# Kernel tuning notes

Measured on AMD Instinct MI355X. Metric: run time of the kernel, lower is better.

## Reference

```python
import jax, jax.numpy as jnp
import numpy as np

CUTOFF = 10.0
K = 32            # max_num_neighbors
NUM_GRAPHS = 64
ATOMS = 128
N = NUM_GRAPHS * ATOMS
HID = 128
FIL = 128
NG = 50           # num_gaussians
LAYERS = 6
MAX_Z = 100
PI = 3.14159265   # constant used verbatim in the torch source


def silu(x):
    return x * jax.nn.sigmoid(x)


def build_graph(pos, batch):
    """Dense cdist + per-node top-K neighbor selection (radius_graph_pure).
    Returns idx[i,k] = k-th nearest neighbor j of center i, and a validity mask.
    Torch edge (row, col) = (j, i): node j receives a message computed from x[i].
    """
    p = jax.lax.stop_gradient(pos)
    d2 = jnp.sum((p[:, None, :] - p[None, :, :]) ** 2, -1)          # [N,N]
    same = batch[:, None] == batch[None, :]
    eye = jnp.eye(p.shape[0], dtype=bool)
    valid = same & (d2 < CUTOFF * CUTOFF) & (~eye)
    dm = jnp.where(valid, d2, jnp.inf)
    neg, idx = jax.lax.top_k(-dm, K)                                 # [N,K]
    return idx, jnp.isfinite(neg)                                    # edge valid iff within mask


def setup_inputs() -> dict:
    key = jax.random.key(0)
    ks = jax.random.split(key, 20)
    s = 0.05
    inp = {
        "pos": jax.random.normal(ks[0], (N, 3), jnp.float32),
        "z": jax.random.randint(ks[1], (N,), 0, MAX_Z),
        "batch": jnp.repeat(jnp.arange(NUM_GRAPHS), ATOMS),
        # parameters (weights stored as [in, out])
        "emb": jax.random.normal(ks[2], (MAX_Z, HID), jnp.float32) * s,
        "mw1": jax.random.normal(ks[3], (LAYERS, NG, FIL), jnp.float32) * s,
        "mb1": jax.random.normal(ks[4], (LAYERS, FIL), jnp.float32) * s,
        "mw2": jax.random.normal(ks[5], (LAYERS, FIL, FIL), jnp.float32) * s,
        "mb2": jax.random.normal(ks[6], (LAYERS, FIL), jnp.float32) * s,
        "l1w": jax.random.normal(ks[7], (LAYERS, HID, FIL), jnp.float32) * s,
        "l1b": jax.random.normal(ks[8], (LAYERS, FIL), jnp.float32) * s,
        "l2w": jax.random.normal(ks[9], (LAYERS, FIL, HID), jnp.float32) * s,
        "l2b": jax.random.normal(ks[10], (LAYERS, HID), jnp.float32) * s,
        "ow1": jax.random.normal(ks[11], (HID, HID // 2), jnp.float32) * s,
        "ob1": jax.random.normal(ks[12], (HID // 2,), jnp.float32) * s,
        "ow2": jax.random.normal(ks[13], (HID // 2, 1), jnp.float32) * s,
        "ob2": jax.random.normal(ks[14], (1,), jnp.float32) * s,
    }
    return inp


def reference(pos, z, batch, emb, mw1, mb1, mw2, mb2, l1w, l1b, l2w, l2b, ow1, ob1, ow2, ob2):
    idx, evalid = build_graph(pos, batch)                 # [N,K], [N,K]
    ev = evalid.astype(pos.dtype)
    diff = pos[idx] - pos[:, None, :]                     # [N,K,3]
    d2e = jnp.sum(diff * diff, -1)
    dist = jnp.sqrt(jnp.where(evalid, d2e, 1.0))          # safe sqrt for masked edges
    offset = jnp.linspace(0.0, CUTOFF, NG)
    width = CUTOFF / (NG - 1)
    rbf = jnp.exp(-0.5 * ((dist[..., None] - offset) / width) ** 2)   # [N,K,NG]
    cval = 0.5 * (jnp.cos(dist * PI / CUTOFF) + 1.0)
    cval = cval * (dist < CUTOFF).astype(pos.dtype) * ev  # zero out invalid edges

    h = emb[z]                                            # [N,HID]
    flat_idx = idx.reshape(-1)                            # receivers (torch row)
    for l in range(LAYERS):
        W = silu(rbf @ mw1[l] + mb1[l]) @ mw2[l] + mb2[l]           # filter MLP
        W = W * cval[..., None]                                       # [N,K,FIL]
        xj = (h @ l1w[l] + l1b[l])[:, None, :]                        # sender = center i
        msg = (xj * W).reshape(N * K, FIL)
        agg = jax.ops.segment_sum(msg, flat_idx, num_segments=N)     # scatter_add at row
        h = h + silu(agg @ l2w[l] + l2b[l])

    out = (silu(h @ ow1 + ob1) @ ow2 + ob2)[:, 0]         # [N]
    return jax.ops.segment_sum(out, batch, num_segments=NUM_GRAPHS)  # [G]
```

## Files before the change

### kernel.cpp

```cpp
#include <hip/hip_runtime.h>
#include <math.h>

typedef unsigned short u16;
typedef unsigned int   u32;
typedef unsigned long long u64;

#define NATOMS 8192
#define GRAPHS 64
#define KNN    32
#define NGAUSS 50
#define HID    128
#define LAYERS 6
#define NTAB   4096
#define SA     136
#define SW1    72
#define SH     132

typedef __attribute__((ext_vector_type(8))) short bf16x8;
typedef __attribute__((ext_vector_type(4))) float f32x4;

__device__ __forceinline__ float bf2f(u16 v) {
    return __uint_as_float(((u32)v) << 16);
}
__device__ __forceinline__ u16 f2bf(float f) {
    u32 u = __float_as_uint(f);
    u32 lsb = (u >> 16) & 1u;
    u += 0x7fffu + lsb;
    return (u16)(u >> 16);
}
__device__ __forceinline__ u32 pkbf(float lo, float hi) {
#if __has_builtin(__builtin_amdgcn_cvt_pk_bf16_f32)
    auto r = __builtin_amdgcn_cvt_pk_bf16_f32(lo, hi);
    u32 u; __builtin_memcpy(&u, &r, 4); return u;
#else
    return (u32)f2bf(lo) | ((u32)f2bf(hi) << 16);
#endif
}
__device__ __forceinline__ float silu_f(float x) {
    return x * __builtin_amdgcn_rcpf(1.0f + __expf(-x));
}
__device__ __forceinline__ bf16x8 ldfrag(const u16* p) {
    return *(const bf16x8*)__builtin_assume_aligned(p, 16);
}
__device__ __forceinline__ u64 shfl_xor_u64(u64 v, int mask) {
    u32 lo = (u32)v, hi = (u32)(v >> 32);
    lo = (u32)__shfl_xor((int)lo, mask, 64);
    hi = (u32)__shfl_xor((int)hi, mask, 64);
    return ((u64)hi << 32) | lo;
}
__device__ __forceinline__ float ldf(const void* p, int i, bool f32in) {
    return f32in ? ((const float*)p)[i] : bf2f(((const u16*)p)[i]);
}
union U8 { bf16x8 v; u32 w[4]; };

__global__ void probe_kernel(const u16* __restrict__ raw, int* __restrict__ flag,
                             int* __restrict__ rev_cnt, float* __restrict__ gsum,
                             int* __restrict__ done_cnt, int* __restrict__ xflags) {
    __shared__ int s;
    int t = threadIdx.x;
    if (t == 0) s = 0;
    __syncthreads();
    float x = bf2f(raw[2 * t]);
    if (!(fabsf(x) < 1000.0f)) atomicOr(&s, 1);
    for (int i = t; i < NATOMS; i += 256) rev_cnt[i] = 0;
    for (int i = t; i < 2048; i += 256) xflags[i] = 0;
    if (t < GRAPHS) gsum[t] = 0.0f;
    if (t == 0) *done_cnt = 0;
    __syncthreads();
    if (t == 0) *flag = s;
}

#define NARR 9
struct IngestDesc {
    const void* src[NARR];
    void*       dst[NARR];
    int         n[NARR];
};

#define NB_BUILD 2048
#define NB_PREP  768

__launch_bounds__(256)
__global__ void setup_kernel(const void* __restrict__ pos,
                             const void* __restrict__ l1w, const void* __restrict__ l2w,
                             u16* __restrict__ l1wt, u16* __restrict__ l2wt,
                             IngestDesc d, int total_ing,
                             const int* __restrict__ flag,
                             int* __restrict__ rev_cnt, u32* __restrict__ rev) {
    int bid = blockIdx.x;
    bool f32in = (*flag != 0);
    if (bid < NB_BUILD) {
        int wv = threadIdx.x >> 6, lane = threadIdx.x & 63;
        int t = bid * 4 + wv;
        int tl = t & 127;
        int base = t & ~127;
        float cx = ldf(pos, t * 3 + 0, f32in);
        float cy = ldf(pos, t * 3 + 1, f32in);
        float cz = ldf(pos, t * 3 + 2, f32in);
        u64 key[2];
#pragma unroll
        for (int c = 0; c < 2; ++c) {
            int j = lane + c * 64;
            float jx = ldf(pos, (base + j) * 3 + 0, f32in);
            float jy = ldf(pos, (base + j) * 3 + 1, f32in);
            float jz = ldf(pos, (base + j) * 3 + 2, f32in);
            float dx = __fsub_rn(cx, jx);
            float dy = __fsub_rn(cy, jy);
            float dz = __fsub_rn(cz, jz);
            float d2 = __fadd_rn(__fadd_rn(__fmul_rn(dx, dx), __fmul_rn(dy, dy)),
                                 __fmul_rn(dz, dz));
            bool valid = (j != tl) && (d2 < 100.0f);
            key[c] = valid ? ((((u64)__float_as_uint(d2)) << 32) | (u32)j) : ~0ULL;
        }
#pragma unroll
        for (int k = 2; k <= 128; k <<= 1) {
#pragma unroll
            for (int j = k >> 1; j > 0; j >>= 1) {
                if (j == 64) {
                    u64 lo = key[0] < key[1] ? key[0] : key[1];
                    u64 hi = key[0] < key[1] ? key[1] : key[0];
                    key[0] = lo; key[1] = hi;
                } else {
#pragma unroll
                    for (int r = 0; r < 2; ++r) {
                        u64 o = shfl_xor_u64(key[r], j);
                        u32 ii = (u32)(r * 64 + lane);
                        bool dir = ((ii & (u32)k) == 0);
                        bool lower = ((ii & (u32)j) == 0);
                        bool keep_min = (dir == lower);
                        bool less = key[r] < o;
                        key[r] = (less == keep_min) ? key[r] : o;
                    }
                }
            }
        }
        if (lane < KNN) {
            u64 m = key[0];
            if (m != ~0ULL) {
                float d2 = __uint_as_float((u32)(m >> 32));
                float dd = __fsqrt_rn(d2);
                if (dd < 10.0f) {
                    float u = dd * ((float)(NTAB - 1) / 10.0f);
                    int i0 = (int)(u + 0.5f);
                    if (i0 > NTAB - 1) i0 = NTAB - 1;
                    int jn = base + (int)(m & 0xffffffffu);
                    int p = atomicAdd(&rev_cnt[jn], 1);
                    rev[(size_t)jn * 128 + p] = ((u32)i0 << 7) | (u32)(t & 127);
                }
            }
        }
    } else if (bid < NB_BUILD + NB_PREP) {
        int gid = (bid - NB_BUILD) * 256 + threadIdx.x;
        int seg = gid / 98304;
        int tt = gid % 98304;
        int l = tt >> 14;
        int n = (tt >> 7) & 127;
        int k = tt & 127;
        const void* src = (seg == 0) ? l1w : l2w;
        u16* dst = (seg == 0) ? l1wt : l2wt;
        int si = l * 16384 + k * 128 + n;
        float v = f32in ? ((const float*)src)[si] : bf2f(((const u16*)src)[si]);
        dst[tt] = f2bf(v);
    } else {
        int gid = (bid - NB_BUILD - NB_PREP) * 256 + threadIdx.x;
        if (gid < total_ing) {
            int a = 0, off = gid;
            while (off >= d.n[a]) { off -= d.n[a]; ++a; }
            float v = f32in ? ((const float*)d.src[a])[off]
                            : bf2f(((const u16*)d.src[a])[off]);
            ((float*)d.dst[a])[off] = v;
        }
    }
}

__launch_bounds__(256)
__global__ void vtab_kernel(const void* __restrict__ mw1,
                            const void* __restrict__ mw2,
                            const float* __restrict__ b1,
                            const float* __restrict__ b2,
                            const int* __restrict__ flag,
                            u32* __restrict__ pk) {
    __shared__ u16 s_t1[128 * SA];
    __shared__ u16 s_w1[128 * SW1];
    __shared__ u16 s_w2[128 * SA];
    int tid = threadIdx.x;
    int l = blockIdx.x / (NTAB / 128);
    int rbase = (blockIdx.x % (NTAB / 128)) * 128;
    {
        bool f32in = (*flag != 0);
#pragma unroll
        for (int p = 0; p < 32; ++p) {
            int idx = p * 256 + tid;
            int k = idx >> 7, n = idx & 127;
            float v = (k < 50) ? ldf(mw1, l * 6400 + k * 128 + n, f32in) : 0.0f;
            s_w1[n * SW1 + k] = f2bf(v);
        }
#pragma unroll
        for (int p = 0; p < 64; ++p) {
            int idx = p * 256 + tid;
            int k = idx >> 7, n = idx & 127;
            s_w2[n * SA + k] = f2bf(ldf(mw2, l * 16384 + k * 128 + n, f32in));
        }
    }
    __syncthreads();

    int wv = tid >> 6, lane = tid & 63;
    int quad = lane >> 4, lr = lane & 15;
    int m0 = wv * 32;

    {
        const float wgi = 49.0f / 10.0f;
        const float dstep = 10.0f / (float)(NTAB - 1);
        U8 afr[2][2];
#pragma unroll
        for (int mt = 0; mt < 2; ++mt) {
            float d = (float)(rbase + m0 + mt * 16 + lr) * dstep;
            float u = d * wgi;
#pragma unroll
            for (int kki = 0; kki < 2; ++kki) {
                float t0 = u - (float)(quad * 8) - (float)(kki * 32);
                float vj[8];
#pragma unroll
                for (int j = 0; j < 8; ++j) {
                    float tt = t0 - (float)j;
                    float e = __expf(-0.5f * tt * tt);
                    if (kki == 1 && (quad * 8 + j) >= 18) e = 0.0f;
                    vj[j] = e;
                }
#pragma unroll
                for (int p = 0; p < 4; ++p)
                    afr[mt][kki].w[p] = pkbf(vj[2 * p], vj[2 * p + 1]);
            }
        }
        f32x4 accA[2][8];
#pragma unroll
        for (int mt = 0; mt < 2; ++mt)
#pragma unroll
            for (int nt = 0; nt < 8; ++nt) accA[mt][nt] = (f32x4){0.f, 0.f, 0.f, 0.f};
#pragma unroll
        for (int kki = 0; kki < 2; ++kki) {
#pragma unroll
            for (int nt = 0; nt < 8; ++nt) {
                bf16x8 b = ldfrag(&s_w1[(nt * 16 + lr) * SW1 + kki * 32 + quad * 8]);
                accA[0][nt] = __builtin_amdgcn_mfma_f32_16x16x32_bf16(afr[0][kki].v, b, accA[0][nt], 0, 0, 0);
                accA[1][nt] = __builtin_amdgcn_mfma_f32_16x16x32_bf16(afr[1][kki].v, b, accA[1][nt], 0, 0, 0);
            }
        }
#pragma unroll
        for (int mt = 0; mt < 2; ++mt) {
            int r0 = m0 + mt * 16 + quad * 4;
            u16* tp0 = &s_t1[r0 * SA + lr];
#pragma unroll
            for (int nt = 0; nt < 8; ++nt) {
                int col = nt * 16;
                float bb = b1[l * 128 + col + lr];
                u32 p01 = pkbf(silu_f(accA[mt][nt][0] + bb),
                               silu_f(accA[mt][nt][1] + bb));
                u32 p23 = pkbf(silu_f(accA[mt][nt][2] + bb),
                               silu_f(accA[mt][nt][3] + bb));
                u16* tp = tp0 + col;
                tp[0]      = (u16)p01;
                tp[SA]     = (u16)(p01 >> 16);
                tp[2 * SA] = (u16)p23;
                tp[3 * SA] = (u16)(p23 >> 16);
            }
        }
    }
    {
        f32x4 accB[2][8];
#pragma unroll
        for (int mt = 0; mt < 2; ++mt)
#pragma unroll
            for (int nt = 0; nt < 8; ++nt) accB[mt][nt] = (f32x4){0.f, 0.f, 0.f, 0.f};
#pragma unroll
        for (int kk = 0; kk < 128; kk += 32) {
            bf16x8 a0 = ldfrag(&s_t1[(m0 + lr)      * SA + kk + quad * 8]);
            bf16x8 a1 = ldfrag(&s_t1[(m0 + 16 + lr) * SA + kk + quad * 8]);
#pragma unroll
            for (int nt = 0; nt < 8; ++nt) {
                bf16x8 b = ldfrag(&s_w2[(nt * 16 + lr) * SA + kk + quad * 8]);
                accB[0][nt] = __builtin_amdgcn_mfma_f32_16x16x32_bf16(a0, b, accB[0][nt], 0, 0, 0);
                accB[1][nt] = __builtin_amdgcn_mfma_f32_16x16x32_bf16(a1, b, accB[1][nt], 0, 0, 0);
            }
        }
        const float dstep = 10.0f / (float)(NTAB - 1);
#pragma unroll
        for (int mt = 0; mt < 2; ++mt) {
            int r0 = m0 + mt * 16 + quad * 4;
            float cv[4];
#pragma unroll
            for (int r = 0; r < 4; ++r) {
                float d = (float)(rbase + r0 + r) * dstep;
                cv[r] = 0.5f * (cosf(d * 3.14159265f / 10.0f) + 1.0f);
            }
#pragma unroll
            for (int nt = 0; nt < 8; ++nt) {
                int col = nt * 16 + lr;
                float bb = b2[l * 128 + col];
#pragma unroll
                for (int r = 0; r < 4; ++r) {
                    float val = (accB[mt][nt][r] + bb) * cv[r];
                    float oth = __shfl_xor(val, 1, 64);
                    if ((lr & 1) == 0) {
                        int row = rbase + r0 + r;
                        pk[((size_t)l * NTAB + row) * 64 + (col >> 1)] =
                            pkbf(val, oth);
                    }
                }
            }
        }
    }
}

#define AGG_ISSUE(T, X, base, ev)                                              \
    {                                                                          \
        _Pragma("unroll") for (int q = 0; q < 8; ++q) {                        \
            int e = (base) + q;                                                \
            u32 pe = __builtin_amdgcn_readlane((ev), e & 63);                  \
            int sy = (int)(pe >> 7);                                           \
            int sx = (int)(pe & 127u);                                         \
            T[q] = pkl[(size_t)sy * 64 + lane];                                \
            X[q] = *(const u32*)&s_x[sx * SA + c2];                            \
        }                                                                      \
    }

#define AGG_COMPUTE(T, X)                                                      \
    {                                                                          \
        _Pragma("unroll") for (int q = 0; q < 8; ++q) {                        \
            float v0 = bf2f((u16)T[q]) * bf2f((u16)X[q]);                      \
            float v1 = bf2f((u16)(T[q] >> 16)) * bf2f((u16)(X[q] >> 16));      \
            switch (q & 3) {                                                   \
                case 0: a0 += v0; a1 += v1; break;                             \
                case 1: b0 += v0; b1v += v1; break;                            \
                case 2: c0 += v0; c1 += v1; break;                             \
                default: d0 += v0; d1 += v1; break;                            \
            }                                                                  \
        }                                                                      \
    }

__launch_bounds__(1024, 1)
__global__ void graph_kernel(const int* __restrict__ rev_cnt,
                             const u32* __restrict__ rev,
                             const u32* __restrict__ pk,
                             const int* __restrict__ z,
                             const float* __restrict__ emb,
                             const u16* __restrict__ l1wt,
                             const float* __restrict__ l1b,
                             const u16* __restrict__ l2wt,
                             const float* __restrict__ l2b,
                             const float* __restrict__ ow1,
                             const float* __restrict__ ob1,
                             const float* __restrict__ ow2,
                             const float* __restrict__ ob2,
                             u32* __restrict__ xbuf,
                             int* __restrict__ xflags,
                             float* __restrict__ gsum,
                             int* __restrict__ done_cnt,
                             void* __restrict__ out,
                             const int* __restrict__ flag) {
    __shared__ __align__(16) u16 s_x[128 * SA];
    __shared__ __align__(16) u16 s_hb[64 * SA];
    __shared__ __align__(16) u16 s_pair[2 * 64 * SA];
    __shared__ float s_b1[128], s_b2[128];
    __shared__ float s_sum;
    __shared__ int s_last;

    u16* s_ahi = s_pair;
    u16* s_alo = s_pair + 64 * SA;

    int tid = threadIdx.x;
    int bid = blockIdx.x;
    int g = bid & 63, q4 = bid >> 6;
    int abase = g * 128;
    int rbase = q4 * 32;
    int w = tid >> 6, lane = tid & 63;
    int quad = lane >> 4, lr = lane & 15;
    int rowt = (w >> 3) * 16;
    int coln = (w & 7) * 16;
    int c2 = lane * 2;

    float hreg[4];

    u32* xb_own[2] = {xbuf + ((size_t)bid * 2 + 0) * 2048,
                      xbuf + ((size_t)bid * 2 + 1) * 2048};

    {
        int r = tid >> 5, cb = (tid & 31) * 4;
        const float* src = emb + (size_t)z[abase + rbase + r] * 128 + cb;
        float4 v = *(const float4*)src;
        u32* dd = (u32*)&s_hb[r * SA + cb];
        dd[0] = pkbf(v.x, v.y); dd[1] = pkbf(v.z, v.w);
    }
    if (tid < 128) s_b1[tid] = l1b[tid];
    __syncthreads();
    {
        f32x4 acc = (f32x4){0.f, 0.f, 0.f, 0.f};
#pragma unroll
        for (int kk = 0; kk < 128; kk += 32) {
            bf16x8 a = ldfrag(&s_hb[(rowt + lr) * SA + kk + quad * 8]);
            bf16x8 b = ldfrag(l1wt + (coln + lr) * 128 + kk + quad * 8);
            acc = __builtin_amdgcn_mfma_f32_16x16x32_bf16(a, b, acc, 0, 0, 0);
        }
#pragma unroll
        for (int r = 0; r < 4; ++r) {
            int col = coln + lr;
            s_x[(rbase + rowt + quad * 4 + r) * SA + col] =
                f2bf(acc[r] + s_b1[col]);
        }
    }

    for (int l = 0; l <= LAYERS; ++l) {
        if (l < LAYERS) {
            int e = l;
            u32* xbw = xb_own[e & 1];
            __syncthreads();
#pragma unroll
            for (int p = 0; p < 2; ++p) {
                int i = tid + p * 1024;
                int row = i >> 6, col = i & 63;
                u32 v = *(const u32*)&s_x[(rbase + row) * SA + col * 2];
                __hip_atomic_store(&xbw[i], v, __ATOMIC_RELAXED,
                                   __HIP_MEMORY_SCOPE_SYSTEM);
            }
            __syncthreads();
            if (tid == 0)
                __hip_atomic_store(&xflags[(g * 4 + q4) * 8 + e], 1,
                                   __ATOMIC_RELAXED, __HIP_MEMORY_SCOPE_SYSTEM);
            if (tid < 3) {
                int pq = (q4 + 1 + tid) & 3;
                const int* pf = &xflags[(g * 4 + pq) * 8 + e];
                while (__hip_atomic_load(pf, __ATOMIC_RELAXED,
                                         __HIP_MEMORY_SCOPE_SYSTEM) == 0)
                    __builtin_amdgcn_s_sleep(8);
            }
            __syncthreads();
#pragma unroll
            for (int k = 0; k < 3; ++k) {
                int pq = (q4 + 1 + k) & 3;
                const u32* xbr = xbuf + ((size_t)(g + 64 * pq) * 2 + (e & 1)) * 2048;
#pragma unroll
                for (int p = 0; p < 2; ++p) {
                    int i = tid + p * 1024;
                    int row = i >> 6, col = i & 63;
                    u32 v = __hip_atomic_load(&xbr[i], __ATOMIC_RELAXED,
                                              __HIP_MEMORY_SCOPE_SYSTEM);
                    *(u32*)&s_x[(pq * 32 + row) * SA + col * 2] = v;
                }
            }
            __syncthreads();
        }
        if (l == LAYERS) break;

        if (tid < 128) {
            s_b2[tid] = l2b[l * 128 + tid];
            if (l < LAYERS - 1) s_b1[tid] = l1b[(l + 1) * 128 + tid];
        }
        const u32* pkl = pk + (size_t)l * NTAB * 64;

        for (int rr = 0; rr < 2; ++rr) {
            int row = w * 2 + rr;
            int j = abase + rbase + row;
            int deg = rev_cnt[j];
            const u32* si = rev + (size_t)j * 128;
            u32 e0 = si[lane];
            u32 e1 = (deg > 64) ? si[64 + lane] : e0;
            float a0 = 0.f, a1 = 0.f, b0 = 0.f, b1v = 0.f;
            float c0 = 0.f, c1 = 0.f, d0 = 0.f, d1 = 0.f;
            u32 tA[8], xA[8], tB[8], xB[8];
            int ng = deg >> 3;
            if (ng > 0) {
                AGG_ISSUE(tA, xA, 0, e0);
                int gi = 1;
                for (; gi + 1 < ng; gi += 2) {
                    u32 evB = (gi < 8) ? e0 : e1;
                    AGG_ISSUE(tB, xB, gi * 8, evB);
                    AGG_COMPUTE(tA, xA);
                    u32 evA = ((gi + 1) < 8) ? e0 : e1;
                    AGG_ISSUE(tA, xA, (gi + 1) * 8, evA);
                    AGG_COMPUTE(tB, xB);
                }
                if (gi < ng) {
                    u32 evB = (gi < 8) ? e0 : e1;
                    AGG_ISSUE(tB, xB, gi * 8, evB);
                    AGG_COMPUTE(tA, xA);
                    AGG_COMPUTE(tB, xB);
                } else {
                    AGG_COMPUTE(tA, xA);
                }
            }
            for (int it = ng * 8; it < deg; ++it) {
                u32 ev = (it < 64) ? e0 : e1;
                u32 pe = __builtin_amdgcn_readlane(ev, it & 63);
                int sy = (int)(pe >> 7);
                int sx = (int)(pe & 127u);
                u32 t = pkl[(size_t)sy * 64 + lane];
                u32 x = *(const u32*)&s_x[sx * SA + c2];
                a0 += bf2f((u16)t) * bf2f((u16)x);
                a1 += bf2f((u16)(t >> 16)) * bf2f((u16)(x >> 16));
            }
            float sxv = (a0 + b0) + (c0 + d0);
            float syv = (a1 + b1v) + (c1 + d1);
            u32 hp = pkbf(sxv, syv);
            u32 lp = pkbf(sxv - bf2f((u16)hp), syv - bf2f((u16)(hp >> 16)));
            *(u32*)&s_ahi[row * SA + c2] = hp;
            *(u32*)&s_alo[row * SA + c2] = lp;
        }
        __syncthreads();

        {
            const u16* B2t = l2wt + (size_t)l * 16384;
            f32x4 acc = (f32x4){0.f, 0.f, 0.f, 0.f};
#pragma unroll
            for (int kk = 0; kk < 128; kk += 32) {
                bf16x8 ah = ldfrag(&s_ahi[(rowt + lr) * SA + kk + quad * 8]);
                bf16x8 al = ldfrag(&s_alo[(rowt + lr) * SA + kk + quad * 8]);
                bf16x8 b = ldfrag(B2t + (coln + lr) * 128 + kk + quad * 8);
                acc = __builtin_amdgcn_mfma_f32_16x16x32_bf16(ah, b, acc, 0, 0, 0);
                acc = __builtin_amdgcn_mfma_f32_16x16x32_bf16(al, b, acc, 0, 0, 0);
            }
            if (l == LAYERS - 1 && tid == 0) s_sum = 0.0f;
#pragma unroll
            for (int r = 0; r < 4; ++r) {
                int row = rowt + quad * 4 + r;
                int col = coln + lr;
                float hold = (l == 0)
                    ? emb[(size_t)z[abase + rbase + row] * 128 + col]
                    : hreg[r];
                float hn = hold + silu_f(acc[r] + s_b2[col]);
                hreg[r] = hn;
                if (l < LAYERS - 1) s_hb[row * SA + col] = f2bf(hn);
            }
        }
        __syncthreads();

        if (l < LAYERS - 1) {
            const u16* B1n = l1wt + (size_t)(l + 1) * 16384;
            f32x4 ac2 = (f32x4){0.f, 0.f, 0.f, 0.f};
#pragma unroll
            for (int kk = 0; kk < 128; kk += 32) {
                bf16x8 a = ldfrag(&s_hb[(rowt + lr) * SA + kk + quad * 8]);
                bf16x8 b = ldfrag(B1n + (coln + lr) * 128 + kk + quad * 8);
                ac2 = __builtin_amdgcn_mfma_f32_16x16x32_bf16(a, b, ac2, 0, 0, 0);
            }
#pragma unroll
            for (int r = 0; r < 4; ++r) {
                int col = coln + lr;
                s_x[(rbase + rowt + quad * 4 + r) * SA + col] =
                    f2bf(ac2[r] + s_b1[col]);
            }
        } else {
            float* s_hf = (float*)s_pair;
            float* s_w  = (float*)s_x;
            {
                float4* dst = (float4*)s_w;
                const float4* src4 = (const float4*)ow1;
                dst[tid] = src4[tid];
                dst[tid + 1024] = src4[tid + 1024];
            }
#pragma unroll
            for (int r = 0; r < 4; ++r)
                s_hf[(rowt + quad * 4 + r) * SH + coln + lr] = hreg[r];
            __syncthreads();
            int atom = tid >> 5, cg = tid & 31;
            const float* hr = &s_hf[atom * SH];
            float ax = 0.f, ay = 0.f;
#pragma unroll 8
            for (int f = 0; f < 128; ++f) {
                float hv = hr[f];
                float2 wv = ((const float2*)&s_w[f * 64])[cg];
                ax += hv * wv.x; ay += hv * wv.y;
            }
            int c0i = cg * 2;
            float v = silu_f(ax + ob1[c0i + 0]) * ow2[c0i + 0]
                    + silu_f(ay + ob1[c0i + 1]) * ow2[c0i + 1];
            v += __shfl_xor(v, 1, 64);
            v += __shfl_xor(v, 2, 64);
            v += __shfl_xor(v, 4, 64);
            v += __shfl_xor(v, 8, 64);
            v += __shfl_xor(v, 16, 64);
            if ((tid & 31) == 0) atomicAdd(&s_sum, v + ob2[0]);
            __syncthreads();
            if (tid == 0) {
                atomicAdd(&gsum[g], s_sum);
                __threadfence();
                int tk = __hip_atomic_fetch_add(done_cnt, 1, __ATOMIC_ACQ_REL,
                                                __HIP_MEMORY_SCOPE_AGENT);
                s_last = (tk == 4 * GRAPHS - 1);
            }
            __syncthreads();
            if (s_last && tid < GRAPHS) {
                float gg = __hip_atomic_load(&gsum[tid], __ATOMIC_RELAXED,
                                             __HIP_MEMORY_SCOPE_AGENT);
                if (*flag) ((float*)out)[tid] = gg;
                else       ((u16*)out)[tid]   = f2bf(gg);
            }
            break;
        }
    }
}

extern "C" void kernel_launch(void* const* d_in, const int* in_sizes, int n_in,
                              void* d_out, int out_size, void* d_ws, size_t ws_size,
                              hipStream_t stream) {
    const void* pos  = d_in[0];
    const int*  z    = (const int*)d_in[1];
    const void* emb  = d_in[3];
    const void* mw1  = d_in[4];
    const void* mb1  = d_in[5];
    const void* mw2  = d_in[6];
    const void* mb2  = d_in[7];
    const void* l1w  = d_in[8];
    const void* l1b  = d_in[9];
    const void* l2w  = d_in[10];
    const void* l2b  = d_in[11];
    const void* ow1  = d_in[12];
    const void* ob1  = d_in[13];
    const void* ow2  = d_in[14];
    const void* ob2  = d_in[15];

    char* ws = (char*)d_ws;
    const size_t KB = 1024, MB = 1048576;
    int*   w_flag  = (int*)  (ws);
    int*   w_done  = (int*)  (ws + 64);
    int*   w_xfl   = (int*)  (ws + 8 * KB);
    float* c_emb   = (float*)(ws + 112 * KB);
    float* c_mb1   = (float*)(ws + 168 * KB);
    float* c_mb2   = (float*)(ws + 176 * KB);
    float* c_l1b   = (float*)(ws + 184 * KB);
    float* c_l2b   = (float*)(ws + 192 * KB);
    float* c_ow1   = (float*)(ws + 200 * KB);
    float* c_ob1   = (float*)(ws + 236 * KB);
    float* c_ow2   = (float*)(ws + 240 * KB);
    float* c_ob2   = (float*)(ws + 244 * KB);
    float* w_gsum  = (float*)(ws + 248 * KB);
    u16*   c_l1wt  = (u16*)  (ws + 256 * KB);
    u16*   c_l2wt  = (u16*)  (ws + 448 * KB);
    int*   rev_cnt = (int*)  (ws + 2  * MB);
    u32*   w_rev   = (u32*)  (ws + 3  * MB);
    u32*   w_pk    = (u32*)  (ws + 21 * MB);
    u32*   w_xbuf  = (u32*)  (ws + 28 * MB);

    probe_kernel<<<1, 256, 0, stream>>>((const u16*)emb, w_flag, rev_cnt,
                                        w_gsum, w_done, w_xfl);

    IngestDesc dsc;
    const void* srcs[NARR] = {emb, mb1, mb2, l1b, l2b, ow1, ob1, ow2, ob2};
    void* dsts[NARR] = {c_emb, c_mb1, c_mb2, c_l1b, c_l2b, c_ow1, c_ob1,
                        c_ow2, c_ob2};
    int ns_[NARR] = {12800, 768, 768, 768, 768, 8192, 64, 64, 1};
    int total = 0;
    for (int a = 0; a < NARR; ++a) {
        dsc.src[a] = srcs[a]; dsc.dst[a] = dsts[a]; dsc.n[a] = ns_[a];
        total += ns_[a];
    }
    int nb_ing = (total + 255) / 256;
    setup_kernel<<<NB_BUILD + NB_PREP + nb_ing, 256, 0, stream>>>(
        pos, l1w, l2w, c_l1wt, c_l2wt, dsc, total, w_flag, rev_cnt, w_rev);

    vtab_kernel<<<LAYERS * NTAB / 128, 256, 0, stream>>>(
        mw1, mw2, c_mb1, c_mb2, w_flag, w_pk);

    graph_kernel<<<4 * GRAPHS, 1024, 0, stream>>>(
        rev_cnt, w_rev, w_pk, z, c_emb, c_l1wt, c_l1b, c_l2wt, c_l2b,
        c_ow1, c_ob1, c_ow2, c_ob2, w_xbuf, w_xfl,
        w_gsum, w_done, d_out, w_flag);
}
```

Baseline: 247.5 us.

## Publish x directly from MFMA epilogue with triple-buffered exchange, hoist bias/neighbor loads

The x = h·l1w + b result is now written straight from the MFMA accumulators to both shared memory and the global exchange buffer, with lane pairs packed via shuffle. This drops the separate copy pass and one block barrier per layer. The exchange buffer becomes triple-buffered, indexed by layer mod 3, which relaxes reuse hazards between peer blocks. All layer biases and each row's reverse-neighbor lists and degrees are loaded once before the layer loop instead of every layer. The cost is extra shared memory for the biases, extra registers for the neighbor indices, and a larger xbuf footprint, which assumes the workspace is big enough for three slots per block.

```diff
diff --git a/kernel.cpp b/kernel.cpp
--- a/kernel.cpp
+++ b/kernel.cpp
@@ -361,7 +361,8 @@
     __shared__ __align__(16) u16 s_x[128 * SA];
     __shared__ __align__(16) u16 s_hb[64 * SA];
     __shared__ __align__(16) u16 s_pair[2 * 64 * SA];
-    __shared__ float s_b1[128], s_b2[128];
+    __shared__ float s_b1a[LAYERS * 128];
+    __shared__ float s_b2a[LAYERS * 128];
     __shared__ float s_sum;
     __shared__ int s_last;
 
@@ -381,8 +382,21 @@
 
     float hreg[4];
 
-    u32* xb_own[2] = {xbuf + ((size_t)bid * 2 + 0) * 2048,
-                      xbuf + ((size_t)bid * 2 + 1) * 2048};
+    for (int i = tid; i < LAYERS * 128; i += 1024) {
+        s_b1a[i] = l1b[i];
+        s_b2a[i] = l2b[i];
+    }
+
+    int j0 = abase + rbase + w * 2;
+    int dgv[2];
+    u32 eAv[2], eBv[2];
+#pragma unroll
+    for (int rr = 0; rr < 2; ++rr) {
+        int j = j0 + rr;
+        dgv[rr] = rev_cnt[j];
+        eAv[rr] = rev[(size_t)j * 128 + lane];
+        eBv[rr] = (dgv[rr] > 64) ? rev[(size_t)j * 128 + 64 + lane] : eAv[rr];
+    }
 
     {
         int r = tid >> 5, cb = (tid & 31) * 4;
@@ -391,8 +405,8 @@
         u32* dd = (u32*)&s_hb[r * SA + cb];
         dd[0] = pkbf(v.x, v.y); dd[1] = pkbf(v.z, v.w);
     }
-    if (tid < 128) s_b1[tid] = l1b[tid];
     __syncthreads();
+
     {
         f32x4 acc = (f32x4){0.f, 0.f, 0.f, 0.f};
 #pragma unroll
@@ -401,69 +415,60 @@
             bf16x8 b = ldfrag(l1wt + (coln + lr) * 128 + kk + quad * 8);
             acc = __builtin_amdgcn_mfma_f32_16x16x32_bf16(a, b, acc, 0, 0, 0);
         }
+        u32* xbw = xbuf + (size_t)bid * 3 * 2048;
+        int col = coln + lr;
 #pragma unroll
         for (int r = 0; r < 4; ++r) {
-            int col = coln + lr;
-            s_x[(rbase + rowt + quad * 4 + r) * SA + col] =
-                f2bf(acc[r] + s_b1[col]);
-        }
-    }
-
-    for (int l = 0; l <= LAYERS; ++l) {
-        if (l < LAYERS) {
-            int e = l;
-            u32* xbw = xb_own[e & 1];
-            __syncthreads();
-#pragma unroll
-            for (int p = 0; p < 2; ++p) {
-                int i = tid + p * 1024;
-                int row = i >> 6, col = i & 63;
-                u32 v = *(const u32*)&s_x[(rbase + row) * SA + col * 2];
-                __hip_atomic_store(&xbw[i], v, __ATOMIC_RELAXED,
-                                   __HIP_MEMORY_SCOPE_SYSTEM);
-            }
-            __syncthreads();
-            if (tid == 0)
-                __hip_atomic_store(&xflags[(g * 4 + q4) * 8 + e], 1,
+            float v = acc[r] + s_b1a[col];
+            float o = __shfl_xor(v, 1, 64);
+            if (!(lr & 1)) {
+                u32 pv = (u32)f2bf(v) | ((u32)f2bf(o) << 16);
+                int row = rowt + quad * 4 + r;
+                *(u32*)&s_x[(rbase + row) * SA + col] = pv;
+                __hip_atomic_store(&xbw[row * 64 + (col >> 1)], pv,
                                    __ATOMIC_RELAXED, __HIP_MEMORY_SCOPE_SYSTEM);
-            if (tid < 3) {
-                int pq = (q4 + 1 + tid) & 3;
-                const int* pf = &xflags[(g * 4 + pq) * 8 + e];
-                while (__hip_atomic_load(pf, __ATOMIC_RELAXED,
-                                         __HIP_MEMORY_SCOPE_SYSTEM) == 0)
-                    __builtin_amdgcn_s_sleep(8);
-            }
-            __syncthreads();
+            }
+        }
+    }
+
+    for (int l = 0; l < LAYERS; ++l) {
+        __syncthreads();
+        if (tid == 0)
+            __hip_atomic_store(&xflags[(g * 4 + q4) * 8 + l], 1,
+                               __ATOMIC_RELAXED, __HIP_MEMORY_SCOPE_SYSTEM);
+        if (tid < 3) {
+            int pq = (q4 + 1 + tid) & 3;
+            const int* pf = &xflags[(g * 4 + pq) * 8 + l];
+            while (__hip_atomic_load(pf, __ATOMIC_RELAXED,
+                                     __HIP_MEMORY_SCOPE_SYSTEM) == 0)
+                __builtin_amdgcn_s_sleep(8);
+        }
+        __syncthreads();
+        {
+            int bufp = l % 3;
 #pragma unroll
             for (int k = 0; k < 3; ++k) {
                 int pq = (q4 + 1 + k) & 3;
-                const u32* xbr = xbuf + ((size_t)(g + 64 * pq) * 2 + (e & 1)) * 2048;
+                const u32* xbr = xbuf + ((size_t)(g + 64 * pq) * 3 + bufp) * 2048;
 #pragma unroll
                 for (int p = 0; p < 2; ++p) {
                     int i = tid + p * 1024;
-                    int row = i >> 6, col = i & 63;
                     u32 v = __hip_atomic_load(&xbr[i], __ATOMIC_RELAXED,
                                               __HIP_MEMORY_SCOPE_SYSTEM);
-                    *(u32*)&s_x[(pq * 32 + row) * SA + col * 2] = v;
-                }
-            }
-            __syncthreads();
-        }
-        if (l == LAYERS) break;
-
-        if (tid < 128) {
-            s_b2[tid] = l2b[l * 128 + tid];
-            if (l < LAYERS - 1) s_b1[tid] = l1b[(l + 1) * 128 + tid];
-        }
+                    *(u32*)&s_x[(pq * 32 + (i >> 6)) * SA + (i & 63) * 2] = v;
+                }
+            }
+        }
+        __syncthreads();
+
         const u32* pkl = pk + (size_t)l * NTAB * 64;
 
+#pragma unroll
         for (int rr = 0; rr < 2; ++rr) {
             int row = w * 2 + rr;
-            int j = abase + rbase + row;
-            int deg = rev_cnt[j];
-            const u32* si = rev + (size_t)j * 128;
-            u32 e0 = si[lane];
-            u32 e1 = (deg > 64) ? si[64 + lane] : e0;
+            int deg = dgv[rr];
+            u32 e0 = eAv[rr];
+            u32 e1 = eBv[rr];
             float a0 = 0.f, a1 = 0.f, b0 = 0.f, b1v = 0.f;
             float c0 = 0.f, c1 = 0.f, d0 = 0.f, d1 = 0.f;
             u32 tA[8], xA[8], tB[8], xB[8];
@@ -519,14 +524,14 @@
                 acc = __builtin_amdgcn_mfma_f32_16x16x32_bf16(al, b, acc, 0, 0, 0);
             }
             if (l == LAYERS - 1 && tid == 0) s_sum = 0.0f;
+            int col = coln + lr;
 #pragma unroll
             for (int r = 0; r < 4; ++r) {
                 int row = rowt + quad * 4 + r;
-                int col = coln + lr;
                 float hold = (l == 0)
                     ? emb[(size_t)z[abase + rbase + row] * 128 + col]
                     : hreg[r];
-                float hn = hold + silu_f(acc[r] + s_b2[col]);
+                float hn = hold + silu_f(acc[r] + s_b2a[l * 128 + col]);
                 hreg[r] = hn;
                 if (l < LAYERS - 1) s_hb[row * SA + col] = f2bf(hn);
             }
@@ -542,11 +547,20 @@
                 bf16x8 b = ldfrag(B1n + (coln + lr) * 128 + kk + quad * 8);
                 ac2 = __builtin_amdgcn_mfma_f32_16x16x32_bf16(a, b, ac2, 0, 0, 0);
             }
+            u32* xbw = xbuf + ((size_t)bid * 3 + ((l + 1) % 3)) * 2048;
+            int col = coln + lr;
 #pragma unroll
             for (int r = 0; r < 4; ++r) {
-                int col = coln + lr;
-                s_x[(rbase + rowt + quad * 4 + r) * SA + col] =
-                    f2bf(ac2[r] + s_b1[col]);
+                float v = ac2[r] + s_b1a[(l + 1) * 128 + col];
+                float o = __shfl_xor(v, 1, 64);
+                if (!(lr & 1)) {
+                    u32 pv = (u32)f2bf(v) | ((u32)f2bf(o) << 16);
+                    int row = rowt + quad * 4 + r;
+                    *(u32*)&s_x[(rbase + row) * SA + col] = pv;
+                    __hip_atomic_store(&xbw[row * 64 + (col >> 1)], pv,
+                                       __ATOMIC_RELAXED,
+                                       __HIP_MEMORY_SCOPE_SYSTEM);
+                }
             }
         } else {
             float* s_hf = (float*)s_pair;
@@ -594,7 +608,6 @@
                 if (*flag) ((float*)out)[tid] = gg;
                 else       ((u16*)out)[tid]   = f2bf(gg);
             }
-            break;
         }
     }
 }
```

Result: slower. 260.3 us (+5.1%).
